# Kernel tuning notes

Hardware: AMD Instinct MI355X
Metric: run time of the kernel (lower is better)

## Reference

```python
import jax, jax.numpy as jnp
import numpy as np

B, S, D = 4, 4096, 2048
G, EPG = 4, 16          # num_groups, experts_per_group
E = G * EPG             # num_experts = 64
H = 64                  # complexity estimator hidden


def setup_inputs() -> dict:
    key = jax.random.key(0)
    ks = jax.random.split(key, 7)
    scale = 0.02
    return {
        "x": jax.random.normal(ks[0], (B, S, D), dtype=jnp.float32),
        "Wg": jax.random.normal(ks[1], (G, D), dtype=jnp.float32) * scale,
        "We": jax.random.normal(ks[2], (G, EPG, D), dtype=jnp.float32) * scale,
        "W1": jax.random.normal(ks[3], (H, D), dtype=jnp.float32) * scale,
        "b1": jax.random.normal(ks[4], (H,), dtype=jnp.float32) * scale,
        "W2": jax.random.normal(ks[5], (1, H), dtype=jnp.float32) * scale,
        "b2": jax.random.normal(ks[6], (1,), dtype=jnp.float32) * scale,
        "min_experts": 1,
        "max_experts": 2,
    }


def _router_forward(x, Wg, We, W1, b1, W2, b2, min_experts, max_experts):
    # complexity estimator: Linear -> ReLU -> Linear -> Sigmoid, squeeze(-1)
    h = jax.nn.relu(jnp.einsum("bsd,hd->bsh", x, W1) + b1)
    complexity = jax.nn.sigmoid(jnp.einsum("bsh,oh->bso", h, W2) + b2)[..., 0]  # [B,S]
    # torch: clamp((score * max_experts).int(), min, max); .int() truncates (floor for >=0)
    k = jnp.clip((complexity * max_experts).astype(jnp.int32), min_experts, max_experts)  # [B,S]

    # group routing
    group_logits = jnp.einsum("bsd,gd->bsg", x, Wg)          # [B,S,G]
    group_probs = jax.nn.softmax(group_logits, axis=-1)
    gidx = jnp.argmax(group_probs, axis=-1)                   # [B,S]

    # per-group expert logits for all groups, then pick the chosen group per token
    expert_logits_all = jnp.einsum("bsd,ged->bsge", x, We)    # [B,S,G,EPG]
    expert_logits = jnp.take_along_axis(
        expert_logits_all, gidx[:, :, None, None], axis=2
    )[:, :, 0, :]                                             # [B,S,EPG]
    expert_probs = jax.nn.softmax(expert_logits, axis=-1)     # [B,S,EPG]

    # per-token top-k (k in {1,2}); always take top-2, mask the 2nd when k==1
    topv, topi = jax.lax.top_k(expert_probs, max_experts)     # [B,S,2]
    use2 = (k >= 2).astype(topv.dtype)                        # [B,S]
    mask = jnp.stack([jnp.ones_like(use2), use2], axis=-1)    # [B,S,2]
    denom = jnp.sum(topv * mask, axis=-1, keepdims=True)
    norm_probs = topv * mask / denom                          # [B,S,2]

    flat_idx = gidx[:, :, None] * EPG + topi                  # [B,S,2] global expert ids
    oh = jax.nn.one_hot(flat_idx, E, dtype=x.dtype)           # [B,S,2,E]
    dispatch = jnp.sum(oh * mask[..., None], axis=2)          # [B,S,E]
    combine = jnp.sum(oh * norm_probs[..., None], axis=2)     # [B,S,E]

    # router_probs: group_prob[gidx] * expert_probs scattered into chosen group's slice
    gp_max = jnp.take_along_axis(group_probs, gidx[..., None], axis=-1)[..., 0]  # [B,S]
    oh_g = jax.nn.one_hot(gidx, G, dtype=x.dtype)             # [B,S,G]
    router_probs = (oh_g[..., :, None] * (gp_max[..., None] * expert_probs)[..., None, :]
                    ).reshape(x.shape[0], x.shape[1], E)      # [B,S,E]

    denom_tok = x.shape[0] * x.shape[1]
    router_prob_per_expert = jnp.sum(router_probs, axis=(0, 1)) / denom_tok
    expert_usage = jnp.sum(dispatch, axis=(0, 1)) / denom_tok
    aux_loss = jnp.sum(router_prob_per_expert * expert_usage) * E
    return dispatch, combine, router_probs, aux_loss


def reference(x, Wg, We, W1, b1, W2, b2, min_experts, max_experts):
    return _router_forward(x, Wg, We, W1, b1, W2, b2, min_experts, max_experts)
```

## Files before the change

### kernel.cpp

```cpp
#include <hip/hip_runtime.h>
#include <cmath>

#define T_TOKENS 16384
#define DIM 2048
#define NG 4
#define EPG 16
#define NE 64
#define NJ2 68
#define NT2 5
#define NJP2 80
#define BM 64
#define KS 4
#define KSL (DIM / KS)
#define NITER (KSL / 32)
#define TAU 0.02f

#define XBUF_B 8192
#define WBUF_B 5120

typedef __attribute__((ext_vector_type(8))) short bf16x8;
typedef __attribute__((ext_vector_type(4))) float f32x4;

#define WF_FLOATS (64 * NT2 * 64 * 4)
#define P_OFF WF_FLOATS
#define P_FLOATS ((size_t)KS * T_TOKENS * NJP2)
#define SUM_OFF (P_OFF + P_FLOATS)
#define CNT_OFF (SUM_OFF + 128)
#define LIST_OFF (CNT_OFF + 4)

static __device__ inline unsigned bf16rne(float x) {
    unsigned u = __float_as_uint(x);
    return (u + 0x7FFFu + ((u >> 16) & 1u)) >> 16;
}

#define GLOAD_LDS(gsrc, ldst) \
    __builtin_amdgcn_global_load_lds( \
        (const __attribute__((address_space(1))) void*)(gsrc), \
        (__attribute__((address_space(3))) void*)(ldst), 16, 0, 0)

__global__ void moe_prep(const float* __restrict__ Wg, const float* __restrict__ We,
                         float* __restrict__ ws, float* __restrict__ sums,
                         int* __restrict__ cnt) {
    int bid = blockIdx.x;
    int kstep = bid / NT2, nt = bid % NT2;
    int lane = threadIdx.x;
    if (bid == 0) {
        sums[lane] = 0.f; sums[64 + lane] = 0.f;
        if (lane == 0) *cnt = 0;
    }
    int row = nt * 16 + (lane & 15);
    int k0 = kstep * 32 + (lane >> 4) * 8;
    const float* src = nullptr;
    if (row < NG)        src = Wg + (size_t)row * DIM;
    else if (row < NJ2)  src = We + (size_t)(row - NG) * DIM;
    unsigned r0 = 0, r1 = 0, r2 = 0, r3 = 0;
    if (src) {
        r0 = bf16rne(src[k0 + 0]) | (bf16rne(src[k0 + 1]) << 16);
        r1 = bf16rne(src[k0 + 2]) | (bf16rne(src[k0 + 3]) << 16);
        r2 = bf16rne(src[k0 + 4]) | (bf16rne(src[k0 + 5]) << 16);
        r3 = bf16rne(src[k0 + 6]) | (bf16rne(src[k0 + 7]) << 16);
    }
    ((uint4*)ws)[(size_t)(kstep * NT2 + nt) * 64 + lane] = make_uint4(r0, r1, r2, r3);
}

__global__ __launch_bounds__(512, 4) void moe_gemm(
    const float* __restrict__ x, const float* __restrict__ wfrag,
    float* __restrict__ part) {
    __shared__ __align__(16) char xs[2][XBUF_B];
    __shared__ __align__(16) char wsb[2][WBUF_B];

    const int bid = blockIdx.x;
    const int tg = bid >> 2, ks = bid & 3;
    const int tid = threadIdx.x;
    const int wave = tid >> 6, lane = tid & 63;
    const int l15 = lane & 15, lq = lane >> 4;
    const int T0 = tg * BM;
    const int K0 = ks * KSL;

    const int xtok = wave * 8 + (lane >> 3);
    const float* xsrc = x + (size_t)(T0 + xtok) * DIM + K0
                      + (((lane & 7) ^ (lane >> 3)) << 2);
    const uint4* wg = (const uint4*)wfrag;

    const int mt = wave & 3, nh = wave >> 2;
    const int ctok = mt * 16 + l15;
    const int csw = ctok & 7;

    f32x4 acc[3];
    acc[0] = (f32x4){0.f,0.f,0.f,0.f};
    acc[1] = (f32x4){0.f,0.f,0.f,0.f};
    acc[2] = (f32x4){0.f,0.f,0.f,0.f};

    auto stage = [&](int it) {
        char* xb = xs[it & 1];
        char* wb = wsb[it & 1];
        GLOAD_LDS(xsrc + it * 32, xb + wave * 1024);
        if (wave < NT2) {
            const int kstep = ks * NITER + it;
            GLOAD_LDS(wg + ((size_t)kstep * NT2 + wave) * 64 + lane, wb + wave * 1024);
        }
    };

    stage(0);
    #pragma unroll 1
    for (int it = 0; it < NITER; ++it) {
        __syncthreads();
        if (it + 1 < NITER) stage(it + 1);
        const char* xb = xs[it & 1];
        const char* wb = wsb[it & 1];

        union { unsigned u[4]; bf16x8 v; } af;
        {
            uint4 lo = *(const uint4*)(xb + ctok * 128 + (((lq * 2) ^ csw) << 4));
            uint4 hi = *(const uint4*)(xb + ctok * 128 + (((lq * 2 + 1) ^ csw) << 4));
            af.u[0] = (lo.x >> 16) | (lo.y & 0xFFFF0000u);
            af.u[1] = (lo.z >> 16) | (lo.w & 0xFFFF0000u);
            af.u[2] = (hi.x >> 16) | (hi.y & 0xFFFF0000u);
            af.u[3] = (hi.z >> 16) | (hi.w & 0xFFFF0000u);
        }
        if (nh == 0) {
            bf16x8 b0 = *(const bf16x8*)(wb + 0 * 1024 + lane * 16);
            bf16x8 b1 = *(const bf16x8*)(wb + 1 * 1024 + lane * 16);
            bf16x8 b2 = *(const bf16x8*)(wb + 2 * 1024 + lane * 16);
            acc[0] = __builtin_amdgcn_mfma_f32_16x16x32_bf16(af.v, b0, acc[0], 0, 0, 0);
            acc[1] = __builtin_amdgcn_mfma_f32_16x16x32_bf16(af.v, b1, acc[1], 0, 0, 0);
            acc[2] = __builtin_amdgcn_mfma_f32_16x16x32_bf16(af.v, b2, acc[2], 0, 0, 0);
        } else {
            bf16x8 b0 = *(const bf16x8*)(wb + 3 * 1024 + lane * 16);
            bf16x8 b1 = *(const bf16x8*)(wb + 4 * 1024 + lane * 16);
            acc[0] = __builtin_amdgcn_mfma_f32_16x16x32_bf16(af.v, b0, acc[0], 0, 0, 0);
            acc[1] = __builtin_amdgcn_mfma_f32_16x16x32_bf16(af.v, b1, acc[1], 0, 0, 0);
        }
    }

    float* po = part + (size_t)ks * T_TOKENS * NJP2
              + (size_t)(T0 + mt * 16 + lq * 4) * NJP2 + l15;
    const int ntb = (nh == 0) ? 0 : 3;
    const int ntn = (nh == 0) ? 3 : 2;
    #pragma unroll
    for (int n = 0; n < 3; ++n) {
        if (n < ntn) {
            #pragma unroll
            for (int r = 0; r < 4; ++r)
                po[(size_t)r * NJP2 + (ntb + n) * 16] = acc[n][r];
        }
    }
}

__global__ __launch_bounds__(256, 4) void moe_epi(
    const float* __restrict__ part, float* __restrict__ out,
    float* __restrict__ sums, int* __restrict__ cnt, int4* __restrict__ list) {
    __shared__ float slog[32][84];
    __shared__ float rp_s[32 * 17];
    __shared__ int   sc_e1[32];
    __shared__ float s_usage[NE], s_rp[NE];

    const int tid = threadIdx.x;
    const int T0 = blockIdx.x * 32;
    if (tid < NE) { s_usage[tid] = 0.f; s_rp[tid] = 0.f; }

    for (int idx = tid; idx < 32 * 20; idx += 256) {
        const int t = idx / 20, q4 = idx % 20;
        const size_t ro = (size_t)(T0 + t) * NJP2 + q4 * 4;
        float4 v = *(const float4*)(part + ro);
        #pragma unroll
        for (int p = 1; p < KS; ++p) {
            float4 u = *(const float4*)(part + (size_t)p * T_TOKENS * NJP2 + ro);
            v.x += u.x; v.y += u.y; v.z += u.z; v.w += u.w;
        }
        *(float4*)&slog[t][q4 * 4] = v;
    }
    __syncthreads();

    #pragma unroll
    for (int half = 0; half < 2; ++half) {
        const int t = (tid >> 4) + half * 16;
        const int q = tid & 15;
        const int tok = T0 + t;
        const float* o = slog[t];

        float gl0 = o[0], gl1 = o[1], gl2 = o[2], gl3 = o[3];
        float gm = gl0; int gi = 0;
        if (gl1 > gm) { gm = gl1; gi = 1; }
        if (gl2 > gm) { gm = gl2; gi = 2; }
        if (gl3 > gm) { gm = gl3; gi = 3; }
        float g2 = -INFINITY;
        if (gi != 0 && gl0 > g2) g2 = gl0;
        if (gi != 1 && gl1 > g2) g2 = gl1;
        if (gi != 2 && gl2 > g2) g2 = gl2;
        if (gi != 3 && gl3 > g2) g2 = gl3;
        bool flagG = (gm - g2) < TAU;
        float gsum = expf(gl0 - gm) + expf(gl1 - gm) + expf(gl2 - gm) + expf(gl3 - gm);
        float gp = 1.f / gsum;

        float el = o[NG + gi * EPG + q];
        float v1v = el; int i1 = q;
        #pragma unroll
        for (int off = 8; off; off >>= 1) {
            float ov = __shfl_xor(v1v, off, 16);
            int   oi = __shfl_xor(i1, off, 16);
            if (ov > v1v || (ov == v1v && oi < i1)) { v1v = ov; i1 = oi; }
        }
        float v2v = (q == i1) ? -INFINITY : el;
        #pragma unroll
        for (int off = 8; off; off >>= 1)
            v2v = fmaxf(v2v, __shfl_xor(v2v, off, 16));
        bool flagE = (v1v - v2v) < TAU;

        float ep = expf(el - v1v);
        float es = ep;
        #pragma unroll
        for (int off = 8; off; off >>= 1) es += __shfl_xor(es, off, 16);
        float inv = 1.f / es;
        rp_s[t * 17 + q] = gp * ep * inv;

        if (q == 0) {
            sc_e1[t] = gi * EPG + i1;
            if (flagG || flagE) {
                int p = atomicAdd(cnt, 1);
                list[p] = make_int4(tok, 0, 0, 0);
            }
        }
    }
    __syncthreads();

    float* outD = out;
    float* outC = out + (size_t)T_TOKENS * NE;
    float* outR = out + (size_t)2 * T_TOKENS * NE;
    for (int idx = tid; idx < 32 * 16; idx += 256) {
        const int t = idx >> 4, f4 = idx & 15;
        const int e0 = f4 * 4;
        const int e1i = sc_e1[t];
        const int gi = e1i >> 4;
        float4 dv, rv;
        float dsum = 0.f, rsum = 0.f;
        {
            float d0 = (e0 + 0 == e1i) ? 1.f : 0.f;
            float d1 = (e0 + 1 == e1i) ? 1.f : 0.f;
            float d2 = (e0 + 2 == e1i) ? 1.f : 0.f;
            float d3 = (e0 + 3 == e1i) ? 1.f : 0.f;
            dv = make_float4(d0, d1, d2, d3);
            dsum = d0 + d1 + d2 + d3;
        }
        {
            bool ing = (e0 >> 4) == gi;
            float r0 = ing ? rp_s[t * 17 + ((e0 + 0) & 15)] : 0.f;
            float r1 = ing ? rp_s[t * 17 + ((e0 + 1) & 15)] : 0.f;
            float r2 = ing ? rp_s[t * 17 + ((e0 + 2) & 15)] : 0.f;
            float r3 = ing ? rp_s[t * 17 + ((e0 + 3) & 15)] : 0.f;
            rv = make_float4(r0, r1, r2, r3);
            rsum = r0 + r1 + r2 + r3;
        }
        const size_t ob = (size_t)(T0 + t) * NE + e0;
        *(float4*)&outD[ob] = dv;
        *(float4*)&outC[ob] = dv;
        *(float4*)&outR[ob] = rv;
        if (dsum != 0.f) atomicAdd(&s_usage[e0 + ((e1i - e0) & 3)], 1.f);
        if (rsum != 0.f) {
            atomicAdd(&s_rp[e0 + 0], rv.x);
            atomicAdd(&s_rp[e0 + 1], rv.y);
            atomicAdd(&s_rp[e0 + 2], rv.z);
            atomicAdd(&s_rp[e0 + 3], rv.w);
        }
    }
    __syncthreads();
    if (tid < NE) {
        atomicAdd(&sums[tid], s_usage[tid]);
        atomicAdd(&sums[NE + tid], s_rp[tid]);
    }
}

__global__ __launch_bounds__(256, 4) void moe_fix(
    const float* __restrict__ x, const float* __restrict__ Wg,
    const float* __restrict__ We, float* __restrict__ out,
    float* __restrict__ sums, const int* __restrict__ cnt,
    const int4* __restrict__ list) {
    __shared__ float gl_s[NG];
    __shared__ float el_s[EPG];
    __shared__ float rp_row[EPG];
    __shared__ int   s_gi, s_e1;
    __shared__ float s_gp;

    const int tid = threadIdx.x;
    const int wave = tid >> 6, lane = tid & 63;
    const int n = *cnt;

    for (int i = blockIdx.x; i < n; i += gridDim.x) {
        const int tok = list[i].x;
        const float* xrow = x + (size_t)tok * DIM;
        float xr[32];
        #pragma unroll
        for (int m = 0; m < 32; ++m) xr[m] = xrow[lane + m * 64];

        auto dotf = [&](const float* w) -> float {
            float s = 0.f;
            #pragma unroll
            for (int m = 0; m < 32; ++m) s = fmaf(xr[m], w[lane + m * 64], s);
            #pragma unroll
            for (int off = 32; off; off >>= 1) s += __shfl_xor(s, off, 64);
            return s;
        };

        {
            float g = dotf(Wg + (size_t)wave * DIM);
            if (lane == 0) gl_s[wave] = g;
        }
        __syncthreads();

        if (tid == 0) {
            float gm = -INFINITY; int gi = 0;
            #pragma unroll
            for (int g = 0; g < NG; ++g)
                if (gl_s[g] > gm) { gm = gl_s[g]; gi = g; }
            float gsum = 0.f;
            #pragma unroll
            for (int g = 0; g < NG; ++g) gsum += expf(gl_s[g] - gm);
            s_gp = 1.f / gsum;
            s_gi = gi;
        }
        __syncthreads();

        const int gi = s_gi;
        for (int j = wave; j < EPG; j += 4) {
            float e = dotf(We + (size_t)(gi * EPG + j) * DIM);
            if (lane == 0) el_s[j] = e;
        }
        __syncthreads();

        if (tid == 0) {
            float e1 = -INFINITY; int i1 = 0;
            #pragma unroll
            for (int j = 0; j < EPG; ++j)
                if (el_s[j] > e1) { e1 = el_s[j]; i1 = j; }
            float es = 0.f;
            #pragma unroll
            for (int j = 0; j < EPG; ++j) {
                float e = expf(el_s[j] - e1);
                rp_row[j] = e;
                es += e;
            }
            float sc = s_gp / es;
            #pragma unroll
            for (int j = 0; j < EPG; ++j) rp_row[j] *= sc;
            s_e1 = gi * EPG + i1;
        }
        __syncthreads();

        if (tid < NE) {
            const int e = tid;
            float newD = (e == s_e1) ? 1.f : 0.f;
            float newR = ((e >> 4) == gi) ? rp_row[e & 15] : 0.f;
            size_t ob = (size_t)tok * NE + e;
            float oldD = out[ob];
            float oldR = out[(size_t)2 * T_TOKENS * NE + ob];
            out[ob] = newD;
            out[(size_t)T_TOKENS * NE + ob] = newD;
            out[(size_t)2 * T_TOKENS * NE + ob] = newR;
            float dD = newD - oldD, dR = newR - oldR;
            if (dD != 0.f) atomicAdd(&sums[e], dD);
            if (dR != 0.f) atomicAdd(&sums[NE + e], dR);
        }
        __syncthreads();
    }
}

__global__ void moe_finalize(const float* __restrict__ sums, float* __restrict__ out) {
    int l = threadIdx.x;
    float v = sums[l] * sums[NE + l];
    #pragma unroll
    for (int off = 32; off; off >>= 1) v += __shfl_down(v, off, 64);
    if (l == 0) {
        float N = (float)T_TOKENS;
        out[(size_t)3 * T_TOKENS * NE] = v * (float)NE / (N * N);
    }
}

extern "C" void kernel_launch(void* const* d_in, const int* in_sizes, int n_in,
                              void* d_out, int out_size, void* d_ws, size_t ws_size,
                              hipStream_t stream) {
    const float* x  = (const float*)d_in[0];
    const float* Wg = (const float*)d_in[1];
    const float* We = (const float*)d_in[2];
    float* out = (float*)d_out;
    float* ws  = (float*)d_ws;

    float* wfrag = ws;
    float* part  = ws + P_OFF;
    float* sums  = ws + SUM_OFF;
    int*   cnt   = (int*)(ws + CNT_OFF);
    int4*  list  = (int4*)(ws + LIST_OFF);

    moe_prep<<<64 * NT2, 64, 0, stream>>>(Wg, We, wfrag, sums, cnt);
    moe_gemm<<<(T_TOKENS / BM) * KS, 512, 0, stream>>>(x, wfrag, part);
    moe_epi<<<T_TOKENS / 32, 256, 0, stream>>>(part, out, sums, cnt, list);
    moe_fix<<<1024, 256, 0, stream>>>(x, Wg, We, out, sums, cnt, list);
    moe_finalize<<<1, 64, 0, stream>>>(sums, out);
}
```

Baseline: 74.77 us.

## Fuse fp32 near-tie recompute into epilogue kernel, dropping separate fix pass

Moves the exact fp32 recomputation for tokens whose bf16 routing decision is near a tie into the epilogue kernel itself. Tokens are flagged in shared memory and recomputed before outputs are written, so the global atomic counter, the token list, the extra kernel launch, and the read-modify-write of outputs and sums are all gone. The cost is that epilogue blocks with flagged tokens serialize a full-row dot product with several barriers, which can cause load imbalance across blocks.

```diff
diff --git a/kernel.cpp b/kernel.cpp
--- a/kernel.cpp
+++ b/kernel.cpp
@@ -25,8 +25,6 @@
 #define P_OFF WF_FLOATS
 #define P_FLOATS ((size_t)KS * T_TOKENS * NJP2)
 #define SUM_OFF (P_OFF + P_FLOATS)
-#define CNT_OFF (SUM_OFF + 128)
-#define LIST_OFF (CNT_OFF + 4)
 
 static __device__ inline unsigned bf16rne(float x) {
     unsigned u = __float_as_uint(x);
@@ -39,15 +37,11 @@
         (__attribute__((address_space(3))) void*)(ldst), 16, 0, 0)
 
 __global__ void moe_prep(const float* __restrict__ Wg, const float* __restrict__ We,
-                         float* __restrict__ ws, float* __restrict__ sums,
-                         int* __restrict__ cnt) {
+                         float* __restrict__ ws, float* __restrict__ sums) {
     int bid = blockIdx.x;
     int kstep = bid / NT2, nt = bid % NT2;
     int lane = threadIdx.x;
-    if (bid == 0) {
-        sums[lane] = 0.f; sums[64 + lane] = 0.f;
-        if (lane == 0) *cnt = 0;
-    }
+    if (bid == 0) { sums[lane] = 0.f; sums[64 + lane] = 0.f; }
     int row = nt * 16 + (lane & 15);
     int k0 = kstep * 32 + (lane >> 4) * 8;
     const float* src = nullptr;
@@ -148,16 +142,23 @@
 }
 
 __global__ __launch_bounds__(256, 4) void moe_epi(
-    const float* __restrict__ part, float* __restrict__ out,
-    float* __restrict__ sums, int* __restrict__ cnt, int4* __restrict__ list) {
+    const float* __restrict__ part, const float* __restrict__ x,
+    const float* __restrict__ Wg, const float* __restrict__ We,
+    float* __restrict__ out, float* __restrict__ sums) {
     __shared__ float slog[32][84];
     __shared__ float rp_s[32 * 17];
     __shared__ int   sc_e1[32];
+    __shared__ char  flagged[32];
     __shared__ float s_usage[NE], s_rp[NE];
+    __shared__ float gl_f[NG], el_f[EPG];
+    __shared__ int   s_gi;
+    __shared__ float s_gp;
 
     const int tid = threadIdx.x;
+    const int wave = tid >> 6, lane = tid & 63;
     const int T0 = blockIdx.x * 32;
     if (tid < NE) { s_usage[tid] = 0.f; s_rp[tid] = 0.f; }
+    if (tid < 32) flagged[tid] = 0;
 
     for (int idx = tid; idx < 32 * 20; idx += 256) {
         const int t = idx / 20, q4 = idx % 20;
@@ -176,7 +177,6 @@
     for (int half = 0; half < 2; ++half) {
         const int t = (tid >> 4) + half * 16;
         const int q = tid & 15;
-        const int tok = T0 + t;
         const float* o = slog[t];
 
         float gl0 = o[0], gl1 = o[1], gl2 = o[2], gl3 = o[3];
@@ -216,13 +216,70 @@
 
         if (q == 0) {
             sc_e1[t] = gi * EPG + i1;
-            if (flagG || flagE) {
-                int p = atomicAdd(cnt, 1);
-                list[p] = make_int4(tok, 0, 0, 0);
+            if (flagG || flagE) flagged[t] = 1;
+        }
+    }
+    __syncthreads();
+
+    for (int t = 0; t < 32; ++t) {
+        if (!flagged[t]) continue;
+        const float* xrow = x + (size_t)(T0 + t) * DIM;
+        float xr[32];
+        #pragma unroll
+        for (int m = 0; m < 32; ++m) xr[m] = xrow[lane + m * 64];
+
+        auto dotf = [&](const float* w) -> float {
+            float s = 0.f;
+            #pragma unroll
+            for (int m = 0; m < 32; ++m) s = fmaf(xr[m], w[lane + m * 64], s);
+            #pragma unroll
+            for (int off = 32; off; off >>= 1) s += __shfl_xor(s, off, 64);
+            return s;
+        };
+
+        {
+            float g = dotf(Wg + (size_t)wave * DIM);
+            if (lane == 0) gl_f[wave] = g;
+        }
+        __syncthreads();
+        if (tid == 0) {
+            float gm = -INFINITY; int gi = 0;
+            #pragma unroll
+            for (int g = 0; g < NG; ++g)
+                if (gl_f[g] > gm) { gm = gl_f[g]; gi = g; }
+            float gsum = 0.f;
+            #pragma unroll
+            for (int g = 0; g < NG; ++g) gsum += expf(gl_f[g] - gm);
+            s_gp = 1.f / gsum;
+            s_gi = gi;
+        }
+        __syncthreads();
+        const int gi = s_gi;
+        #pragma unroll
+        for (int j = 0; j < 4; ++j) {
+            float e = dotf(We + (size_t)(gi * EPG + wave + j * 4) * DIM);
+            if (lane == 0) el_f[wave + j * 4] = e;
+        }
+        __syncthreads();
+        if (tid == 0) {
+            float e1 = -INFINITY; int i1 = 0;
+            #pragma unroll
+            for (int j = 0; j < EPG; ++j)
+                if (el_f[j] > e1) { e1 = el_f[j]; i1 = j; }
+            float es = 0.f;
+            float tmp[EPG];
+            #pragma unroll
+            for (int j = 0; j < EPG; ++j) {
+                float e = expf(el_f[j] - e1);
+                tmp[j] = e; es += e;
             }
-        }
-    }
-    __syncthreads();
+            float sc = s_gp / es;
+            #pragma unroll
+            for (int j = 0; j < EPG; ++j) rp_s[t * 17 + j] = tmp[j] * sc;
+            sc_e1[t] = gi * EPG + i1;
+        }
+        __syncthreads();
+    }
 
     float* outD = out;
     float* outC = out + (size_t)T_TOKENS * NE;
@@ -233,30 +290,27 @@
         const int e1i = sc_e1[t];
         const int gi = e1i >> 4;
         float4 dv, rv;
-        float dsum = 0.f, rsum = 0.f;
         {
             float d0 = (e0 + 0 == e1i) ? 1.f : 0.f;
             float d1 = (e0 + 1 == e1i) ? 1.f : 0.f;
             float d2 = (e0 + 2 == e1i) ? 1.f : 0.f;
             float d3 = (e0 + 3 == e1i) ? 1.f : 0.f;
             dv = make_float4(d0, d1, d2, d3);
-            dsum = d0 + d1 + d2 + d3;
-        }
+        }
+        bool ing = (e0 >> 4) == gi;
         {
-            bool ing = (e0 >> 4) == gi;
             float r0 = ing ? rp_s[t * 17 + ((e0 + 0) & 15)] : 0.f;
             float r1 = ing ? rp_s[t * 17 + ((e0 + 1) & 15)] : 0.f;
             float r2 = ing ? rp_s[t * 17 + ((e0 + 2) & 15)] : 0.f;
             float r3 = ing ? rp_s[t * 17 + ((e0 + 3) & 15)] : 0.f;
             rv = make_float4(r0, r1, r2, r3);
-            rsum = r0 + r1 + r2 + r3;
         }
         const size_t ob = (size_t)(T0 + t) * NE + e0;
         *(float4*)&outD[ob] = dv;
         *(float4*)&outC[ob] = dv;
         *(float4*)&outR[ob] = rv;
-        if (dsum != 0.f) atomicAdd(&s_usage[e0 + ((e1i - e0) & 3)], 1.f);
-        if (rsum != 0.f) {
+        if ((e1i >> 2) == (e0 >> 2)) atomicAdd(&s_usage[e1i], 1.f);
+        if (ing) {
             atomicAdd(&s_rp[e0 + 0], rv.x);
             atomicAdd(&s_rp[e0 + 1], rv.y);
             atomicAdd(&s_rp[e0 + 2], rv.z);
@@ -267,100 +321,6 @@
     if (tid < NE) {
         atomicAdd(&sums[tid], s_usage[tid]);
         atomicAdd(&sums[NE + tid], s_rp[tid]);
-    }
-}
-
-__global__ __launch_bounds__(256, 4) void moe_fix(
-    const float* __restrict__ x, const float* __restrict__ Wg,
-    const float* __restrict__ We, float* __restrict__ out,
-    float* __restrict__ sums, const int* __restrict__ cnt,
-    const int4* __restrict__ list) {
-    __shared__ float gl_s[NG];
-    __shared__ float el_s[EPG];
-    __shared__ float rp_row[EPG];
-    __shared__ int   s_gi, s_e1;
-    __shared__ float s_gp;
-
-    const int tid = threadIdx.x;
-    const int wave = tid >> 6, lane = tid & 63;
-    const int n = *cnt;
-
-    for (int i = blockIdx.x; i < n; i += gridDim.x) {
-        const int tok = list[i].x;
-        const float* xrow = x + (size_t)tok * DIM;
-        float xr[32];
-        #pragma unroll
-        for (int m = 0; m < 32; ++m) xr[m] = xrow[lane + m * 64];
-
-        auto dotf = [&](const float* w) -> float {
-            float s = 0.f;
-            #pragma unroll
-            for (int m = 0; m < 32; ++m) s = fmaf(xr[m], w[lane + m * 64], s);
-            #pragma unroll
-            for (int off = 32; off; off >>= 1) s += __shfl_xor(s, off, 64);
-            return s;
-        };
-
-        {
-            float g = dotf(Wg + (size_t)wave * DIM);
-            if (lane == 0) gl_s[wave] = g;
-        }
-        __syncthreads();
-
-        if (tid == 0) {
-            float gm = -INFINITY; int gi = 0;
-            #pragma unroll
-            for (int g = 0; g < NG; ++g)
-                if (gl_s[g] > gm) { gm = gl_s[g]; gi = g; }
-            float gsum = 0.f;
-            #pragma unroll
-            for (int g = 0; g < NG; ++g) gsum += expf(gl_s[g] - gm);
-            s_gp = 1.f / gsum;
-            s_gi = gi;
-        }
-        __syncthreads();
-
-        const int gi = s_gi;
-        for (int j = wave; j < EPG; j += 4) {
-            float e = dotf(We + (size_t)(gi * EPG + j) * DIM);
-            if (lane == 0) el_s[j] = e;
-        }
-        __syncthreads();
-
-        if (tid == 0) {
-            float e1 = -INFINITY; int i1 = 0;
-            #pragma unroll
-            for (int j = 0; j < EPG; ++j)
-                if (el_s[j] > e1) { e1 = el_s[j]; i1 = j; }
-            float es = 0.f;
-            #pragma unroll
-            for (int j = 0; j < EPG; ++j) {
-                float e = expf(el_s[j] - e1);
-                rp_row[j] = e;
-                es += e;
-            }
-            float sc = s_gp / es;
-            #pragma unroll
-            for (int j = 0; j < EPG; ++j) rp_row[j] *= sc;
-            s_e1 = gi * EPG + i1;
-        }
-        __syncthreads();
-
-        if (tid < NE) {
-            const int e = tid;
-            float newD = (e == s_e1) ? 1.f : 0.f;
-            float newR = ((e >> 4) == gi) ? rp_row[e & 15] : 0.f;
-            size_t ob = (size_t)tok * NE + e;
-            float oldD = out[ob];
-            float oldR = out[(size_t)2 * T_TOKENS * NE + ob];
-            out[ob] = newD;
-            out[(size_t)T_TOKENS * NE + ob] = newD;
-            out[(size_t)2 * T_TOKENS * NE + ob] = newR;
-            float dD = newD - oldD, dR = newR - oldR;
-            if (dD != 0.f) atomicAdd(&sums[e], dD);
-            if (dR != 0.f) atomicAdd(&sums[NE + e], dR);
-        }
-        __syncthreads();
     }
 }
 
@@ -387,12 +347,9 @@
     float* wfrag = ws;
     float* part  = ws + P_OFF;
     float* sums  = ws + SUM_OFF;
-    int*   cnt   = (int*)(ws + CNT_OFF);
-    int4*  list  = (int4*)(ws + LIST_OFF);
-
-    moe_prep<<<64 * NT2, 64, 0, stream>>>(Wg, We, wfrag, sums, cnt);
+
+    moe_prep<<<64 * NT2, 64, 0, stream>>>(Wg, We, wfrag, sums);
     moe_gemm<<<(T_TOKENS / BM) * KS, 512, 0, stream>>>(x, wfrag, part);
-    moe_epi<<<T_TOKENS / 32, 256, 0, stream>>>(part, out, sums, cnt, list);
-    moe_fix<<<1024, 256, 0, stream>>>(x, Wg, We, out, sums, cnt, list);
+    moe_epi<<<T_TOKENS / 32, 256, 0, stream>>>(part, x, Wg, We, out, sums);
     moe_finalize<<<1, 64, 0, stream>>>(sums, out);
 }
```

Result: slower. 101.1 us (+35.2%).
